# Kernel tuning notes

Hardware: AMD Instinct MI355X
Metric: run time of the kernel (lower is better)

## Reference

```python
import jax, jax.numpy as jnp
import numpy as np
import math

B, S, D = 16, 2048, 128

def setup_inputs() -> dict:
    key = jax.random.key(0)
    k1, k2, k3, k4 = jax.random.split(key, 4)
    query = jax.random.normal(k1, (B, S, D), dtype=jnp.float32)
    key_t = jax.random.normal(k2, (B, S, D), dtype=jnp.float32)
    value = jax.random.normal(k3, (B, S, D), dtype=jnp.float32)
    attn_mask = jax.random.randint(k4, (B, S, S), 0, 2).astype(bool)
    return {"query": query, "key": key_t, "value": value, "attn_mask": attn_mask}

def reference(query, key, value, attn_mask):
    # score = Q K^T / sqrt(d)  -> [B, Sq, Sk]
    scale = 1.0 / math.sqrt(query.shape[-1])
    score = jnp.einsum('bqd,bkd->bqk', query, key) * scale
    # faithful quirk: masked positions are replaced by the VALUE 1e-9 (not -inf)
    mask_score = jnp.where(attn_mask, jnp.float32(1e-9), score)
    # faithful quirk: softmax over dim=1 (the query axis), as in the torch source
    score_matrix = jax.nn.softmax(mask_score, axis=1)
    # output = softmax(scores) @ V  -> [B, Sq, D]
    output = jnp.einsum('bqk,bkd->bqd', score_matrix, value)
    return output
```

## Files before the change

### kernel.cpp

```cpp
#include <hip/hip_runtime.h>
#include <math.h>

#define NB 16
#define SS 2048
#define DQ 128
#define SCALE 0.08838834764831845f

typedef __bf16 bf16x8 __attribute__((ext_vector_type(8)));
typedef unsigned short ushort8_t __attribute__((ext_vector_type(8)));
typedef float floatx4 __attribute__((ext_vector_type(4)));

__device__ __forceinline__ unsigned short f2bf(float x) {
  unsigned int u = __float_as_uint(x);
  u += 0x7fffu + ((u >> 16) & 1u);
  return (unsigned short)(u >> 16);
}
union FragU { ushort8_t u; bf16x8 b; };
__device__ __forceinline__ bf16x8 ld_frag(const unsigned short* p) {
  FragU t; t.u = *(const ushort8_t*)p; return t.b;
}
__device__ __forceinline__ floatx4 mfma16(bf16x8 a, bf16x8 b, floatx4 c) {
  return __builtin_amdgcn_mfma_f32_16x16x32_bf16(a, b, c, 0, 0, 0);
}

__device__ __forceinline__ void bar_lds() {
  asm volatile("s_waitcnt lgkmcnt(0)\n\ts_barrier" ::: "memory");
}


__global__ void zero_accum(float* __restrict__ O) {
  float* p = O + (size_t)blockIdx.x * SS * DQ + 16 * DQ;
#pragma unroll
  for (int i = 0; i < 8; ++i) p[threadIdx.x + 256 * i] = 0.f;
}

template<int WRITE_E>
__global__ __launch_bounds__(256, 4) void pass1_colsum(
    const float* __restrict__ Q, const float* __restrict__ K,
    const int* __restrict__ M, float* __restrict__ O,
    unsigned short* __restrict__ E)
{
  const int k0  = blockIdx.x * 64;
  const int b   = blockIdx.y;
  const int qc  = blockIdx.z;
  const int tid = threadIdx.x;
  const int w = tid >> 6, lane = tid & 63, l15 = lane & 15, quad = lane >> 4;

  __shared__ unsigned short Kbf[64][136];
  __shared__ unsigned short Qbf[64][136];
  __shared__ float red[4][64];

  const float* Qb = Q + (size_t)b * SS * DQ;
  const float* Kb = K + (size_t)b * SS * DQ;
  const int*   Mb = M + (size_t)b * SS * SS;
  unsigned short* Eb = WRITE_E ? (E + (size_t)b * SS * SS) : nullptr;

  const int srow = tid >> 5;
  const int sc4  = (tid & 31) * 4;

#pragma unroll
  for (int r = 0; r < 8; ++r) {
    int row = srow + r * 8;
    float4 v = *(const float4*)(Kb + (size_t)(k0 + row) * DQ + sc4);
    *(ushort4*)&Kbf[row][sc4] = make_ushort4(f2bf(v.x), f2bf(v.y), f2bf(v.z), f2bf(v.w));
  }

  const int qlane = 16 * w + l15;

  float4 qreg[8];
  int4 mv_nxt[4];
  {
    const int q0 = qc * 512;
#pragma unroll
    for (int r = 0; r < 8; ++r)
      qreg[r] = *(const float4*)(Qb + (size_t)(q0 + srow + r * 8) * DQ + sc4);
#pragma unroll
    for (int i = 0; i < 4; ++i)
      mv_nxt[i] = *(const int4*)(Mb + (size_t)(q0 + qlane) * SS + k0 + 16 * i + quad * 4);
  }

  float colacc[16];
#pragma unroll
  for (int t = 0; t < 16; ++t) colacc[t] = 0.f;

  for (int qi = 0; qi < 8; ++qi) {
    bar_lds();
    int4 mv[4] = {mv_nxt[0], mv_nxt[1], mv_nxt[2], mv_nxt[3]};
#pragma unroll
    for (int r = 0; r < 8; ++r) {
      float4 v = qreg[r];
      *(ushort4*)&Qbf[srow + r * 8][sc4] =
          make_ushort4(f2bf(v.x), f2bf(v.y), f2bf(v.z), f2bf(v.w));
    }
    bar_lds();
    if (qi < 7) {
      const int qn = qc * 512 + (qi + 1) * 64;
#pragma unroll
      for (int r = 0; r < 8; ++r)
        qreg[r] = *(const float4*)(Qb + (size_t)(qn + srow + r * 8) * DQ + sc4);
#pragma unroll
      for (int i = 0; i < 4; ++i)
        mv_nxt[i] = *(const int4*)(Mb + (size_t)(qn + qlane) * SS + k0 + 16 * i + quad * 4);
    }

    floatx4 acc[4];
#pragma unroll
    for (int i = 0; i < 4; ++i) acc[i] = (floatx4){0.f, 0.f, 0.f, 0.f};
#pragma unroll
    for (int d0 = 0; d0 < DQ; d0 += 32) {
      bf16x8 bq = ld_frag(&Qbf[qlane][d0 + quad * 8]);
#pragma unroll
      for (int i = 0; i < 4; ++i) {
        bf16x8 ak = ld_frag(&Kbf[16 * i + l15][d0 + quad * 8]);
        acc[i] = mfma16(ak, bq, acc[i]);
      }
    }
    const int qrow = qc * 512 + qi * 64 + qlane;
#pragma unroll
    for (int i = 0; i < 4; ++i) {
      int mm[4] = {mv[i].x, mv[i].y, mv[i].z, mv[i].w};
      float ev[4];
#pragma unroll
      for (int r = 0; r < 4; ++r) {
        float s = mm[r] ? 1e-9f : acc[i][r] * SCALE;
        ev[r] = __expf(s);
        colacc[i * 4 + r] += ev[r];
      }
      if (WRITE_E) {
        *(ushort4*)(Eb + (size_t)qrow * SS + k0 + 16 * i + quad * 4) =
            make_ushort4(f2bf(ev[0]), f2bf(ev[1]), f2bf(ev[2]), f2bf(ev[3]));
      }
    }
  }

#pragma unroll
  for (int t = 0; t < 16; ++t) {
    colacc[t] += __shfl_xor(colacc[t], 1, 64);
    colacc[t] += __shfl_xor(colacc[t], 2, 64);
    colacc[t] += __shfl_xor(colacc[t], 4, 64);
    colacc[t] += __shfl_xor(colacc[t], 8, 64);
  }
  if (l15 == 0) {
#pragma unroll
    for (int i = 0; i < 4; ++i)
#pragma unroll
      for (int r = 0; r < 4; ++r)
        red[w][16 * i + quad * 4 + r] = colacc[i * 4 + r];
  }
  bar_lds();
  if (tid < 64) {
    float s = red[0][tid] + red[1][tid] + red[2][tid] + red[3][tid];
    atomicAdd(O + (size_t)b * SS * DQ + 16 * DQ + k0 + tid, s);
  }
}

__global__ void combine_linv(float* __restrict__ O) {
  const int b  = blockIdx.x;
  const int jb = blockIdx.y * 4;
  float* Ob = O + (size_t)b * SS * DQ;
#pragma unroll
  for (int it = 0; it < 8; ++it) {
    int k = threadIdx.x + 256 * it;
    float inv = 1.0f / Ob[16 * DQ + k];
#pragma unroll
    for (int j = 0; j < 4; ++j)
      Ob[(size_t)(64 * (jb + j)) * DQ + k] = inv;
  }
}

__global__ __launch_bounds__(256, 2) void pass2_pv(
    const float* __restrict__ V, const unsigned short* __restrict__ E,
    float* __restrict__ O)
{
  const int b = blockIdx.y, q0 = blockIdx.x * 64;
  const int tid = threadIdx.x;
  const int w = tid >> 6, lane = tid & 63, l15 = lane & 15, quad = lane >> 4;

  __shared__ unsigned short Wt[128][72];
  __shared__ float Li[SS];

  const float* Vb = V + (size_t)b * SS * DQ;
  const unsigned short* Erow =
      E + (size_t)b * SS * SS + (size_t)(q0 + 16 * w + l15) * SS;

  const int sc4 = (tid & 31) * 4;
  const int vk2 = (tid >> 5) * 2;

  {
    const float* src = O + ((size_t)b * SS + q0) * DQ;
#pragma unroll
    for (int r = 0; r < 2; ++r) {
      int idx = (tid + r * 256) * 4;
      *(float4*)&Li[idx] = *(const float4*)(src + idx);
    }
  }

  floatx4 accO[8];
#pragma unroll
  for (int j = 0; j < 8; ++j) accO[j] = (floatx4){0.f, 0.f, 0.f, 0.f};

  float4 vreg[8];
  FragU ef_nxt[2];
  {
#pragma unroll
    for (int r = 0; r < 4; ++r) {
      int k2 = vk2 + r * 16;
      vreg[2 * r]     = *(const float4*)(Vb + (size_t)(k2)     * DQ + sc4);
      vreg[2 * r + 1] = *(const float4*)(Vb + (size_t)(k2 + 1) * DQ + sc4);
    }
#pragma unroll
    for (int c = 0; c < 2; ++c)
      ef_nxt[c].u = *(const ushort8_t*)(Erow + 32 * c + quad * 8);
  }

  for (int k0 = 0; k0 < SS; k0 += 64) {
    bar_lds();
    FragU ef[2] = {ef_nxt[0], ef_nxt[1]};

#pragma unroll
    for (int r = 0; r < 4; ++r) {
      int k2 = vk2 + r * 16;
      float la = Li[k0 + k2], lb = Li[k0 + k2 + 1];
      float fa[4] = {vreg[2*r].x * la, vreg[2*r].y * la,
                     vreg[2*r].z * la, vreg[2*r].w * la};
      float fb[4] = {vreg[2*r+1].x * lb, vreg[2*r+1].y * lb,
                     vreg[2*r+1].z * lb, vreg[2*r+1].w * lb};
#pragma unroll
      for (int i = 0; i < 4; ++i) {
        int d  = sc4 + i;
        int kk = k2 ^ ((((unsigned)d >> 2) & 7) << 3);
        *(ushort2*)&Wt[d][kk] = make_ushort2(f2bf(fa[i]), f2bf(fb[i]));
      }
    }
    bar_lds();

    if (k0 + 64 < SS) {
      const int kn = k0 + 64;
#pragma unroll
      for (int r = 0; r < 4; ++r) {
        int k2 = vk2 + r * 16;
        vreg[2 * r]     = *(const float4*)(Vb + (size_t)(kn + k2)     * DQ + sc4);
        vreg[2 * r + 1] = *(const float4*)(Vb + (size_t)(kn + k2 + 1) * DQ + sc4);
      }
#pragma unroll
      for (int c = 0; c < 2; ++c)
        ef_nxt[c].u = *(const ushort8_t*)(Erow + kn + 32 * c + quad * 8);
    }

#pragma unroll
    for (int c = 0; c < 2; ++c) {
      bf16x8 be = ef[c].b;
#pragma unroll
      for (int j = 0; j < 8; ++j) {
        int d  = 16 * j + l15;
        int kk = (32 * c + quad * 8) ^ ((((unsigned)d >> 2) & 7) << 3);
        bf16x8 aw = ld_frag(&Wt[d][kk]);
        accO[j] = mfma16(aw, be, accO[j]);
      }
    }
  }

#pragma unroll
  for (int j = 0; j < 8; ++j) {
    float* op = O + ((size_t)b * SS + q0 + 16 * w + l15) * DQ + 16 * j + quad * 4;
    *(float4*)op = make_float4(accO[j][0], accO[j][1], accO[j][2], accO[j][3]);
  }
}

__global__ __launch_bounds__(256, 2) void pass2_out(
    const float* __restrict__ Q, const float* __restrict__ K,
    const float* __restrict__ V, const int* __restrict__ M,
    float* __restrict__ O)
{
  const int b = blockIdx.y, q0 = blockIdx.x * 64;
  const int tid = threadIdx.x;
  const int w = tid >> 6, lane = tid & 63, l15 = lane & 15, quad = lane >> 4;

  __shared__ unsigned short Kbf[64][136];
  __shared__ unsigned short Es[64][72];
  __shared__ unsigned short Wt[128][72];
  __shared__ float Li[SS];

  const float* Qb = Q + (size_t)b * SS * DQ;
  const float* Kb = K + (size_t)b * SS * DQ;
  const float* Vb = V + (size_t)b * SS * DQ;
  const int*   Mb = M + (size_t)b * SS * SS;

  const int srow = tid >> 5;
  const int sc4  = (tid & 31) * 4;

  {
    const float* src = O + ((size_t)b * SS + q0) * DQ;
#pragma unroll
    for (int r = 0; r < 2; ++r) {
      int idx = (tid + r * 256) * 4;
      *(float4*)&Li[idx] = *(const float4*)(src + idx);
    }
  }
  FragU qf[4];
  {
    const float* qrow = Qb + (size_t)(q0 + 16 * w + l15) * DQ;
#pragma unroll
    for (int i = 0; i < 4; ++i) {
      float4 a = *(const float4*)(qrow + 32 * i + quad * 8);
      float4 c = *(const float4*)(qrow + 32 * i + quad * 8 + 4);
      qf[i].u = (ushort8_t){f2bf(a.x), f2bf(a.y), f2bf(a.z), f2bf(a.w),
                            f2bf(c.x), f2bf(c.y), f2bf(c.z), f2bf(c.w)};
    }
  }

  floatx4 accO[8];
#pragma unroll
  for (int j = 0; j < 8; ++j) accO[j] = (floatx4){0.f, 0.f, 0.f, 0.f};

  const int* mrow = Mb + (size_t)(q0 + 16 * w + l15) * SS;

  float4 kreg[8], vreg[8];
  int4 mv_nxt[4];
  const int vk2 = (tid >> 5) * 2;
  {
#pragma unroll
    for (int r = 0; r < 8; ++r)
      kreg[r] = *(const float4*)(Kb + (size_t)(srow + r * 8) * DQ + sc4);
#pragma unroll
    for (int r = 0; r < 4; ++r) {
      int k2 = vk2 + r * 16;
      vreg[2 * r]     = *(const float4*)(Vb + (size_t)(k2)     * DQ + sc4);
      vreg[2 * r + 1] = *(const float4*)(Vb + (size_t)(k2 + 1) * DQ + sc4);
    }
#pragma unroll
    for (int j = 0; j < 4; ++j)
      mv_nxt[j] = *(const int4*)(mrow + 16 * j + quad * 4);
  }

  for (int k0 = 0; k0 < SS; k0 += 64) {
    bar_lds();
    int4 mv[4] = {mv_nxt[0], mv_nxt[1], mv_nxt[2], mv_nxt[3]};

#pragma unroll
    for (int r = 0; r < 8; ++r) {
      float4 v = kreg[r];
      *(ushort4*)&Kbf[srow + r * 8][sc4] =
          make_ushort4(f2bf(v.x), f2bf(v.y), f2bf(v.z), f2bf(v.w));
    }
#pragma unroll
    for (int r = 0; r < 4; ++r) {
      int k2 = vk2 + r * 16;
      float fa[4] = {vreg[2*r].x, vreg[2*r].y, vreg[2*r].z, vreg[2*r].w};
      float fb[4] = {vreg[2*r+1].x, vreg[2*r+1].y, vreg[2*r+1].z, vreg[2*r+1].w};
#pragma unroll
      for (int i = 0; i < 4; ++i) {
        int d  = sc4 + i;
        int kk = k2 ^ ((((unsigned)d >> 2) & 7) << 3);
        *(ushort2*)&Wt[d][kk] = make_ushort2(f2bf(fa[i]), f2bf(fb[i]));
      }
    }
    bar_lds();

    if (k0 + 64 < SS) {
      const int kn = k0 + 64;
#pragma unroll
      for (int r = 0; r < 8; ++r)
        kreg[r] = *(const float4*)(Kb + (size_t)(kn + srow + r * 8) * DQ + sc4);
#pragma unroll
      for (int r = 0; r < 4; ++r) {
        int k2 = vk2 + r * 16;
        vreg[2 * r]     = *(const float4*)(Vb + (size_t)(kn + k2)     * DQ + sc4);
        vreg[2 * r + 1] = *(const float4*)(Vb + (size_t)(kn + k2 + 1) * DQ + sc4);
      }
#pragma unroll
      for (int j = 0; j < 4; ++j)
        mv_nxt[j] = *(const int4*)(mrow + kn + 16 * j + quad * 4);
    }

    floatx4 acc[4];
#pragma unroll
    for (int j = 0; j < 4; ++j) acc[j] = (floatx4){0.f, 0.f, 0.f, 0.f};
#pragma unroll
    for (int i = 0; i < 4; ++i) {
      bf16x8 bq = qf[i].b;
#pragma unroll
      for (int j = 0; j < 4; ++j) {
        bf16x8 ak = ld_frag(&Kbf[16 * j + l15][32 * i + quad * 8]);
        acc[j] = mfma16(ak, bq, acc[j]);
      }
    }
#pragma unroll
    for (int j = 0; j < 4; ++j) {
      float4 liv = *(const float4*)&Li[k0 + 16 * j + quad * 4];
      float lv[4] = {liv.x, liv.y, liv.z, liv.w};
      int mm[4] = {mv[j].x, mv[j].y, mv[j].z, mv[j].w};
      unsigned short es[4];
#pragma unroll
      for (int r = 0; r < 4; ++r) {
        float s = mm[r] ? 1e-9f : acc[j][r] * SCALE;
        es[r] = f2bf(__expf(s) * lv[r]);
      }
      *(ushort4*)&Es[16 * w + l15][16 * j + quad * 4] =
          make_ushort4(es[0], es[1], es[2], es[3]);
    }
#pragma unroll
    for (int c = 0; c < 2; ++c) {
      bf16x8 be = ld_frag(&Es[16 * w + l15][32 * c + quad * 8]);
#pragma unroll
      for (int j = 0; j < 8; ++j) {
        int d  = 16 * j + l15;
        int kk = (32 * c + quad * 8) ^ ((((unsigned)d >> 2) & 7) << 3);
        bf16x8 aw = ld_frag(&Wt[d][kk]);
        accO[j] = mfma16(aw, be, accO[j]);
      }
    }
  }

#pragma unroll
  for (int j = 0; j < 8; ++j) {
    float* op = O + ((size_t)b * SS + q0 + 16 * w + l15) * DQ + 16 * j + quad * 4;
    *(float4*)op = make_float4(accO[j][0], accO[j][1], accO[j][2], accO[j][3]);
  }
}

extern "C" void kernel_launch(void* const* d_in, const int* in_sizes, int n_in,
                              void* d_out, int out_size, void* d_ws, size_t ws_size,
                              hipStream_t stream) {
  const float* Q = (const float*)d_in[0];
  const float* K = (const float*)d_in[1];
  const float* V = (const float*)d_in[2];
  const int*   M = (const int*)d_in[3];
  float* O = (float*)d_out;

  const size_t eneed = (size_t)NB * SS * SS * sizeof(unsigned short);

  zero_accum<<<dim3(NB), 256, 0, stream>>>(O);
  if (d_ws != nullptr && ws_size >= eneed) {
    unsigned short* E = (unsigned short*)d_ws;
    pass1_colsum<1><<<dim3(32, NB, 4), 256, 0, stream>>>(Q, K, M, O, E);
    combine_linv<<<dim3(NB, 8), 256, 0, stream>>>(O);
    pass2_pv<<<dim3(32, NB), 256, 0, stream>>>(V, E, O);
  } else {
    pass1_colsum<0><<<dim3(32, NB, 4), 256, 0, stream>>>(Q, K, M, O, nullptr);
    combine_linv<<<dim3(NB, 8), 256, 0, stream>>>(O);
    pass2_out<<<dim3(32, NB), 256, 0, stream>>>(Q, K, V, M, O);
  }
}
```

Measured before the change: 513.5 us.

## Compress mask to bitmask and recompute scores instead of storing exp matrix

Adds a pre-pass that packs the int32 mask into 64-bit ballot words (one bit per element), so later passes read 32x less mask data. Pass 1 no longer writes the bf16 exp matrix. Pass 2 instead recomputes QK^T and the masked exp per tile, scales it by the inverse column sums, and feeds it through LDS into the PV MFMA. This trades the large write and re-read of the bf16 exp matrix for doubled QK^T compute and an extra mask-compression kernel that still reads the full int mask once.

```diff
diff --git a/kernel.cpp b/kernel.cpp
--- a/kernel.cpp
+++ b/kernel.cpp
@@ -9,6 +9,7 @@
 typedef __bf16 bf16x8 __attribute__((ext_vector_type(8)));
 typedef unsigned short ushort8_t __attribute__((ext_vector_type(8)));
 typedef float floatx4 __attribute__((ext_vector_type(4)));
+typedef unsigned long long u64;
 
 __device__ __forceinline__ unsigned short f2bf(float x) {
   unsigned int u = __float_as_uint(x);
@@ -34,11 +35,299 @@
   for (int i = 0; i < 8; ++i) p[threadIdx.x + 256 * i] = 0.f;
 }
 
-template<int WRITE_E>
+__global__ __launch_bounds__(256) void compress_mask(
+    const int* __restrict__ M, u64* __restrict__ Mb)
+{
+  const int b = blockIdx.x;
+  const int q = blockIdx.y * 4 + (threadIdx.x >> 6);
+  const int lane = threadIdx.x & 63;
+
+  const int* row = M + ((size_t)b * SS + q) * SS;
+  int v[32];
+#pragma unroll
+  for (int kt = 0; kt < 32; ++kt) v[kt] = row[kt * 64 + lane];
+
+  u64 w = 0;
+#pragma unroll
+  for (int kt = 0; kt < 32; ++kt) {
+    u64 bal = __ballot(v[kt] != 0);
+    if (lane == kt) w = bal;
+  }
+  u64* orow = Mb + ((size_t)b * SS + q) * 32;
+  if (lane < 32) orow[lane] = w;
+}
+
+__global__ __launch_bounds__(256, 4) void pass1_bits(
+    const float* __restrict__ Q, const float* __restrict__ K,
+    const u64* __restrict__ Mb, float* __restrict__ O)
+{
+  const int kt  = blockIdx.x;
+  const int k0  = kt * 64;
+  const int b   = blockIdx.y;
+  const int qc  = blockIdx.z;
+  const int tid = threadIdx.x;
+  const int w = tid >> 6, lane = tid & 63, l15 = lane & 15, quad = lane >> 4;
+
+  __shared__ unsigned short Kbf[64][136];
+  __shared__ unsigned short Qbf[64][136];
+  __shared__ float red[4][64];
+
+  const float* Qb = Q + (size_t)b * SS * DQ;
+  const float* Kb = K + (size_t)b * SS * DQ;
+  const u64*   Mbb = Mb + (size_t)b * SS * 32 + kt;
+
+  const int srow = tid >> 5;
+  const int sc4  = (tid & 31) * 4;
+
+#pragma unroll
+  for (int r = 0; r < 8; ++r) {
+    int row = srow + r * 8;
+    float4 v = *(const float4*)(Kb + (size_t)(k0 + row) * DQ + sc4);
+    *(ushort4*)&Kbf[row][sc4] = make_ushort4(f2bf(v.x), f2bf(v.y), f2bf(v.z), f2bf(v.w));
+  }
+
+  const int qlane = 16 * w + l15;
+
+  float4 qreg[8];
+  u64 mw_nxt;
+  {
+    const int q0 = qc * 512;
+#pragma unroll
+    for (int r = 0; r < 8; ++r)
+      qreg[r] = *(const float4*)(Qb + (size_t)(q0 + srow + r * 8) * DQ + sc4);
+    mw_nxt = Mbb[(size_t)(q0 + qlane) * 32];
+  }
+
+  float colacc[16];
+#pragma unroll
+  for (int t = 0; t < 16; ++t) colacc[t] = 0.f;
+
+  for (int qi = 0; qi < 8; ++qi) {
+    bar_lds();
+    u64 mw = mw_nxt;
+#pragma unroll
+    for (int r = 0; r < 8; ++r) {
+      float4 v = qreg[r];
+      *(ushort4*)&Qbf[srow + r * 8][sc4] =
+          make_ushort4(f2bf(v.x), f2bf(v.y), f2bf(v.z), f2bf(v.w));
+    }
+    bar_lds();
+    if (qi < 7) {
+      const int qn = qc * 512 + (qi + 1) * 64;
+#pragma unroll
+      for (int r = 0; r < 8; ++r)
+        qreg[r] = *(const float4*)(Qb + (size_t)(qn + srow + r * 8) * DQ + sc4);
+      mw_nxt = Mbb[(size_t)(qn + qlane) * 32];
+    }
+
+    floatx4 acc[4];
+#pragma unroll
+    for (int i = 0; i < 4; ++i) acc[i] = (floatx4){0.f, 0.f, 0.f, 0.f};
+#pragma unroll
+    for (int d0 = 0; d0 < DQ; d0 += 32) {
+      bf16x8 bq = ld_frag(&Qbf[qlane][d0 + quad * 8]);
+#pragma unroll
+      for (int i = 0; i < 4; ++i) {
+        bf16x8 ak = ld_frag(&Kbf[16 * i + l15][d0 + quad * 8]);
+        acc[i] = mfma16(ak, bq, acc[i]);
+      }
+    }
+#pragma unroll
+    for (int i = 0; i < 4; ++i) {
+#pragma unroll
+      for (int r = 0; r < 4; ++r) {
+        int m = (int)(mw >> (16 * i + quad * 4 + r)) & 1;
+        float s = m ? 1e-9f : acc[i][r] * SCALE;
+        colacc[i * 4 + r] += __expf(s);
+      }
+    }
+  }
+
+#pragma unroll
+  for (int t = 0; t < 16; ++t) {
+    colacc[t] += __shfl_xor(colacc[t], 1, 64);
+    colacc[t] += __shfl_xor(colacc[t], 2, 64);
+    colacc[t] += __shfl_xor(colacc[t], 4, 64);
+    colacc[t] += __shfl_xor(colacc[t], 8, 64);
+  }
+  if (l15 == 0) {
+#pragma unroll
+    for (int i = 0; i < 4; ++i)
+#pragma unroll
+      for (int r = 0; r < 4; ++r)
+        red[w][16 * i + quad * 4 + r] = colacc[i * 4 + r];
+  }
+  bar_lds();
+  if (tid < 64) {
+    float s = red[0][tid] + red[1][tid] + red[2][tid] + red[3][tid];
+    atomicAdd(O + (size_t)b * SS * DQ + 16 * DQ + k0 + tid, s);
+  }
+}
+
+__global__ void combine_linv(float* __restrict__ O) {
+  const int b  = blockIdx.x;
+  const int jb = blockIdx.y * 4;
+  float* Ob = O + (size_t)b * SS * DQ;
+#pragma unroll
+  for (int it = 0; it < 8; ++it) {
+    int k = threadIdx.x + 256 * it;
+    float inv = 1.0f / Ob[16 * DQ + k];
+#pragma unroll
+    for (int j = 0; j < 4; ++j)
+      Ob[(size_t)(64 * (jb + j)) * DQ + k] = inv;
+  }
+}
+
+__global__ __launch_bounds__(256, 2) void pass2_bits(
+    const float* __restrict__ Q, const float* __restrict__ K,
+    const float* __restrict__ V, const u64* __restrict__ Mb,
+    float* __restrict__ O)
+{
+  const int b = blockIdx.y, q0 = blockIdx.x * 64;
+  const int tid = threadIdx.x;
+  const int w = tid >> 6, lane = tid & 63, l15 = lane & 15, quad = lane >> 4;
+
+  __shared__ unsigned short Kbf[64][136];
+  __shared__ unsigned short Es[64][72];
+  __shared__ unsigned short Wt[128][72];
+  __shared__ float Li[SS];
+
+  const float* Qb = Q + (size_t)b * SS * DQ;
+  const float* Kb = K + (size_t)b * SS * DQ;
+  const float* Vb = V + (size_t)b * SS * DQ;
+
+  const int srow = tid >> 5;
+  const int sc4  = (tid & 31) * 4;
+
+  {
+    const float* src = O + ((size_t)b * SS + q0) * DQ;
+#pragma unroll
+    for (int r = 0; r < 2; ++r) {
+      int idx = (tid + r * 256) * 4;
+      *(float4*)&Li[idx] = *(const float4*)(src + idx);
+    }
+  }
+  FragU qf[4];
+  {
+    const float* qrow = Qb + (size_t)(q0 + 16 * w + l15) * DQ;
+#pragma unroll
+    for (int i = 0; i < 4; ++i) {
+      float4 a = *(const float4*)(qrow + 32 * i + quad * 8);
+      float4 c = *(const float4*)(qrow + 32 * i + quad * 8 + 4);
+      qf[i].u = (ushort8_t){f2bf(a.x), f2bf(a.y), f2bf(a.z), f2bf(a.w),
+                            f2bf(c.x), f2bf(c.y), f2bf(c.z), f2bf(c.w)};
+    }
+  }
+
+  floatx4 accO[8];
+#pragma unroll
+  for (int j = 0; j < 8; ++j) accO[j] = (floatx4){0.f, 0.f, 0.f, 0.f};
+
+  const u64* brow = Mb + (size_t)(b * SS + q0 + 16 * w + l15) * 32;
+
+  float4 kreg[8], vreg[8];
+  u64 mw_nxt;
+  const int vk2 = (tid >> 5) * 2;
+  {
+#pragma unroll
+    for (int r = 0; r < 8; ++r)
+      kreg[r] = *(const float4*)(Kb + (size_t)(srow + r * 8) * DQ + sc4);
+#pragma unroll
+    for (int r = 0; r < 4; ++r) {
+      int k2 = vk2 + r * 16;
+      vreg[2 * r]     = *(const float4*)(Vb + (size_t)(k2)     * DQ + sc4);
+      vreg[2 * r + 1] = *(const float4*)(Vb + (size_t)(k2 + 1) * DQ + sc4);
+    }
+    mw_nxt = brow[0];
+  }
+
+  for (int k0 = 0; k0 < SS; k0 += 64) {
+    bar_lds();
+    u64 mw = mw_nxt;
+
+#pragma unroll
+    for (int r = 0; r < 8; ++r) {
+      float4 v = kreg[r];
+      *(ushort4*)&Kbf[srow + r * 8][sc4] =
+          make_ushort4(f2bf(v.x), f2bf(v.y), f2bf(v.z), f2bf(v.w));
+    }
+#pragma unroll
+    for (int r = 0; r < 4; ++r) {
+      int k2 = vk2 + r * 16;
+      float fa[4] = {vreg[2*r].x, vreg[2*r].y, vreg[2*r].z, vreg[2*r].w};
+      float fb[4] = {vreg[2*r+1].x, vreg[2*r+1].y, vreg[2*r+1].z, vreg[2*r+1].w};
+#pragma unroll
+      for (int i = 0; i < 4; ++i) {
+        int d  = sc4 + i;
+        int kk = k2 ^ ((((unsigned)d >> 2) & 7) << 3);
+        *(ushort2*)&Wt[d][kk] = make_ushort2(f2bf(fa[i]), f2bf(fb[i]));
+      }
+    }
+    bar_lds();
+
+    if (k0 + 64 < SS) {
+      const int kn = k0 + 64;
+#pragma unroll
+      for (int r = 0; r < 8; ++r)
+        kreg[r] = *(const float4*)(Kb + (size_t)(kn + srow + r * 8) * DQ + sc4);
+#pragma unroll
+      for (int r = 0; r < 4; ++r) {
+        int k2 = vk2 + r * 16;
+        vreg[2 * r]     = *(const float4*)(Vb + (size_t)(kn + k2)     * DQ + sc4);
+        vreg[2 * r + 1] = *(const float4*)(Vb + (size_t)(kn + k2 + 1) * DQ + sc4);
+      }
+      mw_nxt = brow[(kn >> 6)];
+    }
+
+    floatx4 acc[4];
+#pragma unroll
+    for (int j = 0; j < 4; ++j) acc[j] = (floatx4){0.f, 0.f, 0.f, 0.f};
+#pragma unroll
+    for (int i = 0; i < 4; ++i) {
+      bf16x8 bq = qf[i].b;
+#pragma unroll
+      for (int j = 0; j < 4; ++j) {
+        bf16x8 ak = ld_frag(&Kbf[16 * j + l15][32 * i + quad * 8]);
+        acc[j] = mfma16(ak, bq, acc[j]);
+      }
+    }
+#pragma unroll
+    for (int j = 0; j < 4; ++j) {
+      float4 liv = *(const float4*)&Li[k0 + 16 * j + quad * 4];
+      float lv[4] = {liv.x, liv.y, liv.z, liv.w};
+      unsigned short es[4];
+#pragma unroll
+      for (int r = 0; r < 4; ++r) {
+        int m = (int)(mw >> (16 * j + quad * 4 + r)) & 1;
+        float s = m ? 1e-9f : acc[j][r] * SCALE;
+        es[r] = f2bf(__expf(s) * lv[r]);
+      }
+      *(ushort4*)&Es[16 * w + l15][16 * j + quad * 4] =
+          make_ushort4(es[0], es[1], es[2], es[3]);
+    }
+#pragma unroll
+    for (int c = 0; c < 2; ++c) {
+      bf16x8 be = ld_frag(&Es[16 * w + l15][32 * c + quad * 8]);
+#pragma unroll
+      for (int j = 0; j < 8; ++j) {
+        int d  = 16 * j + l15;
+        int kk = (32 * c + quad * 8) ^ ((((unsigned)d >> 2) & 7) << 3);
+        bf16x8 aw = ld_frag(&Wt[d][kk]);
+        accO[j] = mfma16(aw, be, accO[j]);
+      }
+    }
+  }
+
+#pragma unroll
+  for (int j = 0; j < 8; ++j) {
+    float* op = O + ((size_t)b * SS + q0 + 16 * w + l15) * DQ + 16 * j + quad * 4;
+    *(float4*)op = make_float4(accO[j][0], accO[j][1], accO[j][2], accO[j][3]);
+  }
+}
+
 __global__ __launch_bounds__(256, 4) void pass1_colsum(
     const float* __restrict__ Q, const float* __restrict__ K,
-    const int* __restrict__ M, float* __restrict__ O,
-    unsigned short* __restrict__ E)
+    const int* __restrict__ M, float* __restrict__ O)
 {
   const int k0  = blockIdx.x * 64;
   const int b   = blockIdx.y;
@@ -53,7 +342,6 @@
   const float* Qb = Q + (size_t)b * SS * DQ;
   const float* Kb = K + (size_t)b * SS * DQ;
   const int*   Mb = M + (size_t)b * SS * SS;
-  unsigned short* Eb = WRITE_E ? (E + (size_t)b * SS * SS) : nullptr;
 
   const int srow = tid >> 5;
   const int sc4  = (tid & 31) * 4;
@@ -115,20 +403,13 @@
         acc[i] = mfma16(ak, bq, acc[i]);
       }
     }
-    const int qrow = qc * 512 + qi * 64 + qlane;
 #pragma unroll
     for (int i = 0; i < 4; ++i) {
       int mm[4] = {mv[i].x, mv[i].y, mv[i].z, mv[i].w};
-      float ev[4];
 #pragma unroll
       for (int r = 0; r < 4; ++r) {
         float s = mm[r] ? 1e-9f : acc[i][r] * SCALE;
-        ev[r] = __expf(s);
-        colacc[i * 4 + r] += ev[r];
-      }
-      if (WRITE_E) {
-        *(ushort4*)(Eb + (size_t)qrow * SS + k0 + 16 * i + quad * 4) =
-            make_ushort4(f2bf(ev[0]), f2bf(ev[1]), f2bf(ev[2]), f2bf(ev[3]));
+        colacc[i * 4 + r] += __expf(s);
       }
     }
   }
@@ -151,119 +432,6 @@
   if (tid < 64) {
     float s = red[0][tid] + red[1][tid] + red[2][tid] + red[3][tid];
     atomicAdd(O + (size_t)b * SS * DQ + 16 * DQ + k0 + tid, s);
-  }
-}
-
-__global__ void combine_linv(float* __restrict__ O) {
-  const int b  = blockIdx.x;
-  const int jb = blockIdx.y * 4;
-  float* Ob = O + (size_t)b * SS * DQ;
-#pragma unroll
-  for (int it = 0; it < 8; ++it) {
-    int k = threadIdx.x + 256 * it;
-    float inv = 1.0f / Ob[16 * DQ + k];
-#pragma unroll
-    for (int j = 0; j < 4; ++j)
-      Ob[(size_t)(64 * (jb + j)) * DQ + k] = inv;
-  }
-}
-
-__global__ __launch_bounds__(256, 2) void pass2_pv(
-    const float* __restrict__ V, const unsigned short* __restrict__ E,
-    float* __restrict__ O)
-{
-  const int b = blockIdx.y, q0 = blockIdx.x * 64;
-  const int tid = threadIdx.x;
-  const int w = tid >> 6, lane = tid & 63, l15 = lane & 15, quad = lane >> 4;
-
-  __shared__ unsigned short Wt[128][72];
-  __shared__ float Li[SS];
-
-  const float* Vb = V + (size_t)b * SS * DQ;
-  const unsigned short* Erow =
-      E + (size_t)b * SS * SS + (size_t)(q0 + 16 * w + l15) * SS;
-
-  const int sc4 = (tid & 31) * 4;
-  const int vk2 = (tid >> 5) * 2;
-
-  {
-    const float* src = O + ((size_t)b * SS + q0) * DQ;
-#pragma unroll
-    for (int r = 0; r < 2; ++r) {
-      int idx = (tid + r * 256) * 4;
-      *(float4*)&Li[idx] = *(const float4*)(src + idx);
-    }
-  }
-
-  floatx4 accO[8];
-#pragma unroll
-  for (int j = 0; j < 8; ++j) accO[j] = (floatx4){0.f, 0.f, 0.f, 0.f};
-
-  float4 vreg[8];
-  FragU ef_nxt[2];
-  {
-#pragma unroll
-    for (int r = 0; r < 4; ++r) {
-      int k2 = vk2 + r * 16;
-      vreg[2 * r]     = *(const float4*)(Vb + (size_t)(k2)     * DQ + sc4);
-      vreg[2 * r + 1] = *(const float4*)(Vb + (size_t)(k2 + 1) * DQ + sc4);
-    }
-#pragma unroll
-    for (int c = 0; c < 2; ++c)
-      ef_nxt[c].u = *(const ushort8_t*)(Erow + 32 * c + quad * 8);
-  }
-
-  for (int k0 = 0; k0 < SS; k0 += 64) {
-    bar_lds();
-    FragU ef[2] = {ef_nxt[0], ef_nxt[1]};
-
-#pragma unroll
-    for (int r = 0; r < 4; ++r) {
-      int k2 = vk2 + r * 16;
-      float la = Li[k0 + k2], lb = Li[k0 + k2 + 1];
-      float fa[4] = {vreg[2*r].x * la, vreg[2*r].y * la,
-                     vreg[2*r].z * la, vreg[2*r].w * la};
-      float fb[4] = {vreg[2*r+1].x * lb, vreg[2*r+1].y * lb,
-                     vreg[2*r+1].z * lb, vreg[2*r+1].w * lb};
-#pragma unroll
-      for (int i = 0; i < 4; ++i) {
-        int d  = sc4 + i;
-        int kk = k2 ^ ((((unsigned)d >> 2) & 7) << 3);
-        *(ushort2*)&Wt[d][kk] = make_ushort2(f2bf(fa[i]), f2bf(fb[i]));
-      }
-    }
-    bar_lds();
-
-    if (k0 + 64 < SS) {
-      const int kn = k0 + 64;
-#pragma unroll
-      for (int r = 0; r < 4; ++r) {
-        int k2 = vk2 + r * 16;
-        vreg[2 * r]     = *(const float4*)(Vb + (size_t)(kn + k2)     * DQ + sc4);
-        vreg[2 * r + 1] = *(const float4*)(Vb + (size_t)(kn + k2 + 1) * DQ + sc4);
-      }
-#pragma unroll
-      for (int c = 0; c < 2; ++c)
-        ef_nxt[c].u = *(const ushort8_t*)(Erow + kn + 32 * c + quad * 8);
-    }
-
-#pragma unroll
-    for (int c = 0; c < 2; ++c) {
-      bf16x8 be = ef[c].b;
-#pragma unroll
-      for (int j = 0; j < 8; ++j) {
-        int d  = 16 * j + l15;
-        int kk = (32 * c + quad * 8) ^ ((((unsigned)d >> 2) & 7) << 3);
-        bf16x8 aw = ld_frag(&Wt[d][kk]);
-        accO[j] = mfma16(aw, be, accO[j]);
-      }
-    }
-  }
-
-#pragma unroll
-  for (int j = 0; j < 8; ++j) {
-    float* op = O + ((size_t)b * SS + q0 + 16 * w + l15) * DQ + 16 * j + quad * 4;
-    *(float4*)op = make_float4(accO[j][0], accO[j][1], accO[j][2], accO[j][3]);
   }
 }
 
@@ -428,16 +596,17 @@
   const int*   M = (const int*)d_in[3];
   float* O = (float*)d_out;
 
-  const size_t eneed = (size_t)NB * SS * SS * sizeof(unsigned short);
+  const size_t bneed = (size_t)NB * SS * 32 * sizeof(u64);
 
   zero_accum<<<dim3(NB), 256, 0, stream>>>(O);
-  if (d_ws != nullptr && ws_size >= eneed) {
-    unsigned short* E = (unsigned short*)d_ws;
-    pass1_colsum<1><<<dim3(32, NB, 4), 256, 0, stream>>>(Q, K, M, O, E);
+  if (d_ws != nullptr && ws_size >= bneed) {
+    u64* Mb = (u64*)d_ws;
+    compress_mask<<<dim3(NB, 512), 256, 0, stream>>>(M, Mb);
+    pass1_bits<<<dim3(32, NB, 4), 256, 0, stream>>>(Q, K, Mb, O);
     combine_linv<<<dim3(NB, 8), 256, 0, stream>>>(O);
-    pass2_pv<<<dim3(32, NB), 256, 0, stream>>>(V, E, O);
+    pass2_bits<<<dim3(32, NB), 256, 0, stream>>>(Q, K, V, Mb, O);
   } else {
-    pass1_colsum<0><<<dim3(32, NB, 4), 256, 0, stream>>>(Q, K, M, O, nullptr);
+    pass1_colsum<<<dim3(32, NB, 4), 256, 0, stream>>>(Q, K, M, O);
     combine_linv<<<dim3(NB, 8), 256, 0, stream>>>(O);
     pass2_out<<<dim3(32, NB), 256, 0, stream>>>(Q, K, V, M, O);
   }
```

Result: slower. 535.2 us (+4.2%).
